# Optimization experiments

Measured on AMD Instinct MI355X. Metric: run time of the kernel, lower is better.

Reference implementation:

```python
import jax, jax.numpy as jnp
import numpy as np

NL, H, N, CIN, COUT, B, L = 4, 256, 64, 64, 8, 8, 1024
LN_EPS = 1e-5


def layernorm(x, w, b):
    m = x.mean(-1, keepdims=True)
    v = ((x - m) ** 2).mean(-1, keepdims=True)
    return (x - m) / jnp.sqrt(v + LN_EPS) * w + b


def s4d(u, A, C, D, log_step):
    # u: [B, H, L] real; A: [N] complex; C: [H, N] complex
    Lq = u.shape[-1]
    step = jnp.exp(log_step)                       # [H]
    dA = step[:, None] * A[None, :]                # [H, N] complex
    C_bar = C * (jnp.exp(dA) - 1.0) / A[None, :]   # [H, N]
    l = jnp.arange(Lq, dtype=jnp.float32)
    P = jnp.exp(l[:, None, None] * dA[None])       # [L, H, N] complex (dominant intermediate)
    K = jnp.einsum('hn,lhn->hl', C_bar, P)         # [H, L] complex
    kf = jnp.fft.rfft(K.real, n=2 * Lq) + 1j * jnp.fft.rfft(K.imag, n=2 * Lq)  # [H, L+1]
    uf = jnp.fft.rfft(u, n=2 * Lq)                 # [B, H, L+1]
    y = jnp.fft.irfft(kf * uf, n=2 * Lq)[..., :Lq]  # [B, H, L] real
    return y + u * D[:, None]


def forward(stimulus_seq, initial_state, A_re, A_im, C_re, C_im, D, log_step,
            ln1_w, ln1_b, ln2_w, ln2_b, W1, b1, W2, b2,
            Win, b_in, Wst, b_st, Wout, b_out):
    # stimulus_seq: [B, CIN, L] -> [B, L, CIN]
    x = stimulus_seq.transpose(0, 2, 1) @ Win.T + b_in            # [B, L, H]
    x = x + (initial_state @ Wst.T + b_st)[:, None, :]            # fusion_mode='add'
    for i in range(NL):
        xn = layernorm(x, ln1_w[i], ln1_b[i])
        A = A_re[i] + 1j * A_im[i]
        C = C_re[i] + 1j * C_im[i]
        y = s4d(xn.transpose(0, 2, 1), A, C, D[i], log_step[i])
        x = x + y.transpose(0, 2, 1)
        xn = layernorm(x, ln2_w[i], ln2_b[i])
        h = jax.nn.gelu(xn @ W1[i].T + b1[i], approximate=False)  # torch GELU = exact erf
        x = x + h @ W2[i].T + b2[i]
    out = x @ Wout.T + b_out                                      # [B, L, COUT]
    # use_voltage_filter=False: split + concat is identity on channel axis
    return out.transpose(0, 2, 1)                                 # [B, COUT, L]


def setup_inputs() -> dict:
    key = jax.random.key(0)
    ks = iter(jax.random.split(key, 24))
    def u(shape, fan_in):
        lim = 1.0 / np.sqrt(fan_in)
        return jax.random.uniform(next(ks), shape, minval=-lim, maxval=lim, dtype=jnp.float32)
    inp = {
        'stimulus_seq': jax.random.normal(next(ks), (B, CIN, L), dtype=jnp.float32),
        'initial_state': jax.random.normal(next(ks), (B, COUT), dtype=jnp.float32),
        'A_re': -0.5 * jnp.ones((NL, N), dtype=jnp.float32),
        'A_im': jnp.tile(jnp.arange(N, dtype=jnp.float32) * np.float32(np.pi), (NL, 1)),
        'C_re': jax.random.normal(next(ks), (NL, H, N), dtype=jnp.float32),
        'C_im': jax.random.normal(next(ks), (NL, H, N), dtype=jnp.float32),
        'D': jax.random.normal(next(ks), (NL, H), dtype=jnp.float32),
        'log_step': jax.random.uniform(next(ks), (NL, H), dtype=jnp.float32) * np.float32(np.log(0.1) - np.log(1e-4)) + np.float32(np.log(1e-4)),
        'ln1_w': jnp.ones((NL, H), dtype=jnp.float32),
        'ln1_b': jnp.zeros((NL, H), dtype=jnp.float32),
        'ln2_w': jnp.ones((NL, H), dtype=jnp.float32),
        'ln2_b': jnp.zeros((NL, H), dtype=jnp.float32),
        'W1': u((NL, 2 * H, H), H), 'b1': u((NL, 2 * H), H),
        'W2': u((NL, H, 2 * H), 2 * H), 'b2': u((NL, H), 2 * H),
        'Win': u((H, CIN), CIN), 'b_in': u((H,), CIN),
        'Wst': u((H, COUT), COUT), 'b_st': u((H,), COUT),
        'Wout': u((COUT, H), H), 'b_out': u((COUT,), H),
    }
    return inp


def reference(stimulus_seq, initial_state, A_re, A_im, C_re, C_im, D, log_step,
              ln1_w, ln1_b, ln2_w, ln2_b, W1, b1, W2, b2,
              Win, b_in, Wst, b_st, Wout, b_out):
    return forward(stimulus_seq, initial_state, A_re, A_im, C_re, C_im, D, log_step,
                   ln1_w, ln1_b, ln2_w, ln2_b, W1, b1, W2, b2,
                   Win, b_in, Wst, b_st, Wout, b_out)
```

## Files before the change

### kernel.cpp

```cpp
#include <hip/hip_runtime.h>
#include <math.h>

#define NL   4
#define H    256
#define NST  64
#define CIN  64
#define COUT 8
#define BB   8
#define LL   1024
#define NFFT 2048

typedef __attribute__((ext_vector_type(8))) short bf16x8;
typedef __attribute__((ext_vector_type(4))) short short4v;
typedef __attribute__((ext_vector_type(4))) int   int4v;
typedef __attribute__((ext_vector_type(4))) float f32x4;

__device__ __forceinline__ short f2bf(float f) {
  union { float f; unsigned u; } v; v.f = f;
  unsigned r = (v.u + 0x7fffu + ((v.u >> 16) & 1u)) >> 16;
  return (short)r;
}
__device__ __forceinline__ int IDX2(int a) { return a + (a >> 4); }
#define FBUF 2176

__device__ __forceinline__ float2 cadd(float2 a, float2 b) { return make_float2(a.x + b.x, a.y + b.y); }
__device__ __forceinline__ float2 csub(float2 a, float2 b) { return make_float2(a.x - b.x, a.y - b.y); }

template <int SGN>
__device__ __forceinline__ void bfly8(const float2 a[8], float2 A[8]) {
  const float RH = 0.70710678118654752f;
  float2 s0 = cadd(a[0], a[4]), s1 = csub(a[0], a[4]);
  float2 s2 = cadd(a[2], a[6]), s3 = csub(a[2], a[6]);
  float2 mi = (SGN < 0) ? make_float2(s3.y, -s3.x) : make_float2(-s3.y, s3.x);
  float2 E0 = cadd(s0, s2), E1 = cadd(s1, mi), E2 = csub(s0, s2), E3 = csub(s1, mi);
  float2 t0 = cadd(a[1], a[5]), t1 = csub(a[1], a[5]);
  float2 t2 = cadd(a[3], a[7]), t3 = csub(a[3], a[7]);
  float2 mj = (SGN < 0) ? make_float2(t3.y, -t3.x) : make_float2(-t3.y, t3.x);
  float2 O0 = cadd(t0, t2), O1 = cadd(t1, mj), O2 = csub(t0, t2), O3 = csub(t1, mj);
  float2 W0 = O0;
  float2 W1 = (SGN < 0) ? make_float2((O1.x + O1.y) * RH, (O1.y - O1.x) * RH)
                        : make_float2((O1.x - O1.y) * RH, (O1.x + O1.y) * RH);
  float2 W2 = (SGN < 0) ? make_float2(O2.y, -O2.x) : make_float2(-O2.y, O2.x);
  float2 W3 = (SGN < 0) ? make_float2((O3.y - O3.x) * RH, -(O3.x + O3.y) * RH)
                        : make_float2(-(O3.x + O3.y) * RH, (O3.x - O3.y) * RH);
  A[0] = cadd(E0, W0); A[4] = csub(E0, W0);
  A[1] = cadd(E1, W1); A[5] = csub(E1, W1);
  A[2] = cadd(E2, W2); A[6] = csub(E2, W2);
  A[3] = cadd(E3, W3); A[7] = csub(E3, W3);
}

template <int SGN>
__device__ __forceinline__ void fft_stage0_reg(const float2 a[8], float2* d,
                                               const float2* __restrict__ tw, int tid) {
  float2 A[8];
  bfly8<SGN>(a, A);
  const int base = 8 * tid;
  d[IDX2(base)] = A[0];
#pragma unroll
  for (int dd = 1; dd < 8; ++dd) {
    float2 w = tw[dd * tid];
    float wi = (SGN < 0) ? w.y : -w.y;
    d[IDX2(base + dd)] = make_float2(A[dd].x * w.x - A[dd].y * wi,
                                     A[dd].x * wi + A[dd].y * w.x);
  }
}

template <int SGN>
__device__ __forceinline__ void fft_stage0_reg_tw(const float2 a[8], float2* d,
                                                  const float2 w[7], int tid) {
  float2 A[8];
  bfly8<SGN>(a, A);
  const int base = 8 * tid;
  d[IDX2(base)] = A[0];
#pragma unroll
  for (int dd = 1; dd < 8; ++dd) {
    float wr = w[dd - 1].x;
    float wi = (SGN < 0) ? w[dd - 1].y : -w[dd - 1].y;
    d[IDX2(base + dd)] = make_float2(A[dd].x * wr - A[dd].y * wi,
                                     A[dd].x * wi + A[dd].y * wr);
  }
}

template <int SGN>
__device__ __forceinline__ void fft_mid_stages(float2* bA, float2* bB,
                                               const float2* __restrict__ tw, int tid) {
#pragma unroll
  for (int st = 1; st < 3; ++st) {
    float2* s = (st == 1) ? bA : bB;
    float2* d = (st == 1) ? bB : bA;
    const int m = 1 << (3 * st);
    __syncthreads();
    const int k  = tid & (m - 1);
    const int jm = tid - k;
    float2 a[8], A[8];
#pragma unroll
    for (int q = 0; q < 8; ++q) a[q] = s[IDX2(tid + 256 * q)];
    bfly8<SGN>(a, A);
    const int base = 8 * jm + k;
    d[IDX2(base)] = A[0];
#pragma unroll
    for (int dd = 1; dd < 8; ++dd) {
      float2 w = tw[dd * jm];
      float wi = (SGN < 0) ? w.y : -w.y;
      d[IDX2(base + dd * m)] = make_float2(A[dd].x * w.x - A[dd].y * wi,
                                           A[dd].x * wi + A[dd].y * w.x);
    }
  }
}

template <int SGN>
__device__ __forceinline__ void fft_final_r4_lds(const float2* s, float2* d, int tid) {
  __syncthreads();
#pragma unroll
  for (int q = 0; q < 2; ++q) {
    const int t = tid + (q << 8);
    float2 x0 = s[IDX2(t)], x1 = s[IDX2(t + 512)];
    float2 x2 = s[IDX2(t + 1024)], x3 = s[IDX2(t + 1536)];
    float2 s0 = cadd(x0, x2), s1 = csub(x0, x2);
    float2 s2 = cadd(x1, x3), s3 = csub(x1, x3);
    float2 mi = (SGN < 0) ? make_float2(s3.y, -s3.x) : make_float2(-s3.y, s3.x);
    d[IDX2(t)]        = cadd(s0, s2);
    d[IDX2(t + 512)]  = cadd(s1, mi);
    d[IDX2(t + 1024)] = csub(s0, s2);
    d[IDX2(t + 1536)] = csub(s1, mi);
  }
  __syncthreads();
}

template <int SGN>
__device__ __forceinline__ void fft_final_r4_reg(const float2* s, int tid,
                                                 float2 out0[4], float2 out1[4]) {
  __syncthreads();
#pragma unroll
  for (int q = 0; q < 2; ++q) {
    const int t = tid + (q << 8);
    float2 x0 = s[IDX2(t)], x1 = s[IDX2(t + 512)];
    float2 x2 = s[IDX2(t + 1024)], x3 = s[IDX2(t + 1536)];
    float2 s0 = cadd(x0, x2), s1 = csub(x0, x2);
    float2 s2 = cadd(x1, x3), s3 = csub(x1, x3);
    float2 mi = (SGN < 0) ? make_float2(s3.y, -s3.x) : make_float2(-s3.y, s3.x);
    float2* o = q ? out1 : out0;
    o[0] = cadd(s0, s2);
    o[1] = cadd(s1, mi);
    o[2] = csub(s0, s2);
    o[3] = csub(s1, mi);
  }
}

__global__ __launch_bounds__(256) void k_setup(
    const float* __restrict__ W1, const float* __restrict__ W2, const float* __restrict__ Win,
    const float* __restrict__ init, const float* __restrict__ Wst,
    const float* __restrict__ bst, const float* __restrict__ bin,
    short* __restrict__ W1s, short* __restrict__ W2s, float* __restrict__ WinT,
    float* __restrict__ sp, float2* __restrict__ tw) {
  int idx = blockIdx.x * 256 + threadIdx.x;
  if (idx < 2048) {
    float s, c;
    sincosf(3.14159265358979323846f * (float)idx / 1024.0f, &s, &c);
    tw[idx] = make_float2(c, -s);
  }
  if (idx < 65536) {
    int i = idx >> 14, c = idx & 16383;
    int cblk = c >> 11, s = (c >> 8) & 7, n = (c >> 6) & 3, lane = c & 63;
    int cl = lane & 15, rg = lane >> 4;
    int col = cblk * 64 + n * 16 + cl;
    const float* srcp = W1 + ((size_t)(i * 512 + col)) * 256 + s * 32 + rg * 8;
    short* dstp = W1s + ((size_t)idx) * 8;
#pragma unroll
    for (int j = 0; j < 8; ++j) dstp[j] = f2bf(srcp[j]);
  } else if (idx < 131072) {
    int t = idx - 65536;
    int i = t >> 14, c = t & 16383;
    int cblk = c >> 11, s = (c >> 7) & 15, n = (c >> 6) & 1, lane = c & 63;
    int cl = lane & 15, rg = lane >> 4;
    int col = cblk * 32 + n * 16 + cl;
    const float* srcp = W2 + ((size_t)(i * 256 + col)) * 512 + s * 32 + rg * 8;
    short* dstp = W2s + ((size_t)t) * 8;
#pragma unroll
    for (int j = 0; j < 8; ++j) dstp[j] = f2bf(srcp[j]);
  }
  if (idx < 256 * 64) {
    int hh = idx / 64, c = idx % 64;
    WinT[c * 256 + hh] = Win[idx];
  }
  if (idx < BB * H) {
    int b = idx >> 8, h = idx & 255;
    float acc = bin[h] + bst[h];
#pragma unroll
    for (int c = 0; c < COUT; ++c) acc += init[b * COUT + c] * Wst[h * COUT + c];
    sp[idx] = acc;
  }
}

__global__ __launch_bounds__(256) void k_in_ln1(
    const float* __restrict__ stim, const float* __restrict__ WinT,
    const float* __restrict__ sp, const float* __restrict__ lw, const float* __restrict__ lb,
    float* __restrict__ x, float* __restrict__ xnT) {
  int blk = blockIdx.x;
  int b_ = blk >> 6, l0 = (blk & 63) << 4;
  int tid = threadIdx.x, wv = tid >> 6, lane = tid & 63;
  __shared__ float sc[16][CIN];
  __shared__ float T[16][256];
#pragma unroll
  for (int it = 0; it < 4; ++it) {
    int idx = tid + (it << 8);
    int r = idx & 15, c = idx >> 4;
    sc[r][c] = stim[(b_ * CIN + c) * LL + l0 + r];
  }
  __syncthreads();
  float4 sp4 = *(const float4*)&sp[b_ * H + lane * 4];
  float4 acc[4] = {sp4, sp4, sp4, sp4};
  for (int c = 0; c < CIN; ++c) {
    float4 wv4 = *(const float4*)&WinT[c * H + lane * 4];
#pragma unroll
    for (int rr = 0; rr < 4; ++rr) {
      float s = sc[wv * 4 + rr][c];
      acc[rr].x += s * wv4.x; acc[rr].y += s * wv4.y;
      acc[rr].z += s * wv4.z; acc[rr].w += s * wv4.w;
    }
  }
  float4 w4 = *(const float4*)&lw[lane * 4];
  float4 c4 = *(const float4*)&lb[lane * 4];
#pragma unroll
  for (int rr = 0; rr < 4; ++rr) {
    int lr = wv * 4 + rr;
    float4 v = acc[rr];
    *(float4*)&x[(((size_t)(b_ << 10) + l0 + lr)) * H + lane * 4] = v;
    float s = v.x + v.y + v.z + v.w;
#pragma unroll
    for (int o = 32; o > 0; o >>= 1) s += __shfl_xor(s, o, 64);
    float m = s * (1.0f / H);
    float dx = v.x - m, dy = v.y - m, dz = v.z - m, dw = v.w - m;
    float q = dx * dx + dy * dy + dz * dz + dw * dw;
#pragma unroll
    for (int o = 32; o > 0; o >>= 1) q += __shfl_xor(q, o, 64);
    float rs = rsqrtf(q * (1.0f / H) + 1e-5f);
    float4 o4;
    o4.x = dx * rs * w4.x + c4.x; o4.y = dy * rs * w4.y + c4.y;
    o4.z = dz * rs * w4.z + c4.z; o4.w = dw * rs * w4.w + c4.w;
    *(float4*)&T[lr][lane * 4] = o4;
  }
  __syncthreads();
  float tmp[16];
#pragma unroll
  for (int l = 0; l < 16; ++l) tmp[l] = T[l][tid];
  float* dst = xnT + ((size_t)(b_ * H + tid)) * LL + l0;
#pragma unroll
  for (int l = 0; l < 16; l += 4) {
    float4 v = {tmp[l], tmp[l + 1], tmp[l + 2], tmp[l + 3]};
    *(float4*)&dst[l] = v;
  }
}

__global__ __launch_bounds__(256) void k_kernelfft(
    const float* __restrict__ A_re, const float* __restrict__ A_im,
    const float* __restrict__ C_re, const float* __restrict__ C_im,
    const float* __restrict__ log_step, const float2* __restrict__ tw,
    float2* __restrict__ kf) {
  int blk = blockIdx.x;
  int i = blk >> 8;
  int tid = threadIdx.x;
  __shared__ float2 cb[NST], Mv[NST];
  __shared__ float2 bufA[FBUF], bufB[FBUF];
  float2* T1 = bufB;
  float2* T2 = bufB + 1024;
  float step = expf(log_step[blk]);
  int n = tid & 63, g = tid >> 6;
  float Ar = A_re[i * NST + n], Ai = A_im[i * NST + n];
  float dr = step * Ar, di = step * Ai;
  float er = expf(dr);
  float sn, cs; sincosf(di, &sn, &cs);
  float Er = er * cs, Ei = er * sn;
  if (g == 0) {
    float nr = Er - 1.0f, ni = Ei;
    float dnm = Ar * Ar + Ai * Ai;
    float qr = (nr * Ar + ni * Ai) / dnm;
    float qi = (ni * Ar - nr * Ai) / dnm;
    float Cr = C_re[(size_t)blk * NST + n], Ci = C_im[(size_t)blk * NST + n];
    cb[n] = make_float2(Cr * qr - Ci * qi, Cr * qi + Ci * qr);
    float pr = 1.f, pi = 0.f;
    T1[n * 16] = make_float2(1.f, 0.f);
    for (int a = 1; a < 16; ++a) {
      float t2 = pr * Er - pi * Ei; pi = pr * Ei + pi * Er; pr = t2;
      T1[n * 16 + a] = make_float2(pr, pi);
    }
  } else if (g == 1) {
    float xr = Er, xi = Ei;
#pragma unroll
    for (int j = 0; j < 4; ++j) { float t2 = xr * xr - xi * xi; xi = 2.f * xr * xi; xr = t2; }
    float pr = 1.f, pi = 0.f;
    T2[n * 16] = make_float2(1.f, 0.f);
    for (int a = 1; a < 16; ++a) {
      float t2 = pr * xr - pi * xi; pi = pr * xi + pi * xr; pr = t2;
      T2[n * 16 + a] = make_float2(pr, pi);
    }
    float mr2 = pr * xr - pi * xi, mi2 = pr * xi + pi * xr;
    Mv[n] = make_float2(mr2, mi2);
  }
  __syncthreads();
  float kr[4] = {0.f, 0.f, 0.f, 0.f}, ki[4] = {0.f, 0.f, 0.f, 0.f};
  const int a_lo = tid & 15, a_hi = tid >> 4;
  for (int nn = 0; nn < NST; ++nn) {
    float2 t1 = T1[nn * 16 + a_lo];
    float2 t2v = T2[nn * 16 + a_hi];
    float pr = t1.x * t2v.x - t1.y * t2v.y;
    float pi = t1.x * t2v.y + t1.y * t2v.x;
    float2 c = cb[nn], m = Mv[nn];
#pragma unroll
    for (int q = 0; q < 4; ++q) {
      kr[q] += c.x * pr - c.y * pi;
      ki[q] += c.x * pi + c.y * pr;
      float t2 = pr * m.x - pi * m.y;
      pi = pr * m.y + pi * m.x;
      pr = t2;
    }
  }
  float2 a[8];
#pragma unroll
  for (int q = 0; q < 4; ++q) a[q] = make_float2(kr[q], ki[q]);
  a[4] = a[5] = a[6] = a[7] = make_float2(0.f, 0.f);
  fft_stage0_reg<-1>(a, bufA, tw, tid);
  fft_mid_stages<-1>(bufA, bufB, tw, tid);
  float2 F0[4], F1[4];
  fft_final_r4_reg<-1>(bufA, tid, F0, F1);
  float2* kfh = kf + (size_t)blk * 1025;
  kfh[tid]       = F0[0];
  kfh[tid + 512] = F0[1];
  kfh[tid + 256] = F1[0];
  kfh[tid + 768] = F1[1];
  if (tid == 0) kfh[1024] = F0[2];
}

__global__ __launch_bounds__(256) void k_conv(
    const float* __restrict__ xnT, const float2* __restrict__ kf,
    const float* __restrict__ D, const float2* __restrict__ tw, float* __restrict__ yT) {
  int blk = blockIdx.x;
  int b_ = blk >> 7, hp = blk & 127;
  int h0 = hp * 2, h1 = h0 + 1;
  int r0 = b_ * H + h0;
  int tid = threadIdx.x;
  __shared__ float2 bufA[FBUF], bufB[FBUF];
  float2 w0[7];
#pragma unroll
  for (int dd = 1; dd < 8; ++dd) w0[dd - 1] = tw[dd * tid];
  float u0[4], u1[4];
  const float* x0 = xnT + (size_t)r0 * LL;
  const float* x1 = x0 + LL;
  float2 a[8];
#pragma unroll
  for (int q = 0; q < 4; ++q) {
    int l = tid + (q << 8);
    float v0 = x0[l], v1 = x1[l];
    u0[q] = v0; u1[q] = v1;
    a[q] = make_float2(v0, v1);
  }
  a[4] = a[5] = a[6] = a[7] = make_float2(0.f, 0.f);
  fft_stage0_reg_tw<-1>(a, bufA, w0, tid);
  fft_mid_stages<-1>(bufA, bufB, tw, tid);
  fft_final_r4_lds<-1>(bufA, bufB, tid);
  const float2* kf0 = kf + (size_t)h0 * 1025;
  const float2* kf1 = kf + (size_t)h1 * 1025;
#pragma unroll
  for (int q = 0; q < 4; ++q) {
    int k = tid + (q << 8);
    if (k == 0) {
      float2 k0 = kf0[0], k1 = kf1[0];
      float2 F0 = bufB[IDX2(0)], Fn = bufB[IDX2(1024)];
      bufA[IDX2(0)]    = make_float2(F0.x * k0.x, F0.y * k1.x);
      float2 k0n = kf0[1024], k1n = kf1[1024];
      bufA[IDX2(1024)] = make_float2(Fn.x * k0n.x, Fn.y * k1n.x);
    } else {
      float2 F = bufB[IDX2(k)], G = bufB[IDX2(2048 - k)];
      float u0r = 0.5f * (F.x + G.x), u0i = 0.5f * (F.y - G.y);
      float dr_ = 0.5f * (F.x - G.x), di_ = 0.5f * (F.y + G.y);
      float u1r = di_, u1i = -dr_;
      float2 k0 = kf0[k], k1 = kf1[k];
      float z0r = u0r * k0.x - u0i * k0.y, z0i = u0r * k0.y + u0i * k0.x;
      float z1r = u1r * k1.x - u1i * k1.y, z1i = u1r * k1.y + u1i * k1.x;
      bufA[IDX2(k)]        = make_float2(z0r - z1i, z0i + z1r);
      bufA[IDX2(2048 - k)] = make_float2(z0r + z1i, z1r - z0i);
    }
  }
  __syncthreads();
  float2 g[8];
#pragma unroll
  for (int q = 0; q < 8; ++q) g[q] = bufA[IDX2(tid + 256 * q)];
  fft_stage0_reg_tw<1>(g, bufB, w0, tid);
  fft_mid_stages<1>(bufB, bufA, tw, tid);
  float2 z0[4], z1[4];
  fft_final_r4_reg<1>(bufB, tid, z0, z1);
  float Dh0 = D[h0], Dh1 = D[h1];
  float* y0 = yT + (size_t)r0 * LL;
  float* y1 = y0 + LL;
  const float s = 1.0f / NFFT;
  y0[tid]       = z0[0].x * s + Dh0 * u0[0];
  y0[tid + 256] = z1[0].x * s + Dh0 * u0[1];
  y0[tid + 512] = z0[1].x * s + Dh0 * u0[2];
  y0[tid + 768] = z1[1].x * s + Dh0 * u0[3];
  y1[tid]       = z0[0].y * s + Dh1 * u1[0];
  y1[tid + 256] = z1[0].y * s + Dh1 * u1[1];
  y1[tid + 512] = z0[1].y * s + Dh1 * u1[2];
  y1[tid + 768] = z1[1].y * s + Dh1 * u1[3];
}

#define TXS 260
template <bool LAST>
__global__ __launch_bounds__(512, 4) void k_mlp(
    const short* __restrict__ W1p, const float* __restrict__ b1p,
    const short* __restrict__ W2p, const float* __restrict__ b2p,
    float* __restrict__ x, const float* __restrict__ yT,
    const float* __restrict__ ln2w, const float* __restrict__ ln2b,
    const float* __restrict__ ln1w, const float* __restrict__ ln1b,
    float* __restrict__ xnT,
    const float* __restrict__ Wout, const float* __restrict__ bout,
    float* __restrict__ out) {
  const int m0 = blockIdx.x * 16;
  const int b_ = m0 >> 10, l0 = m0 & 1023;
  const int tid = threadIdx.x;
  const int lane = tid & 63, wid = tid >> 6;
  const int rg = lane >> 4, cl = lane & 15;
  __shared__ __attribute__((aligned(16))) char smem[26112];
  short* A1  = (short*)smem;
  short* A2  = (short*)(smem + 8448);
  float* red = (float*)(smem + 25088);
  float* Txn = (float*)smem;
  float* wlds = (float*)(smem + 16896);

  const short* w1base = W1p + (size_t)wid * 16384 + lane * 8;
  bf16x8 pre[4];
#pragma unroll
  for (int n = 0; n < 4; ++n)
    pre[n] = *(const bf16x8*)(w1base + n * 512);

  float v[2][4];
  float wl2[2], bl2[2];
#pragma unroll
  for (int n = 0; n < 2; ++n) {
    int col = wid * 32 + n * 16 + cl;
    wl2[n] = ln2w[col]; bl2[n] = ln2b[col];
  }
  float sum[4], sq[4];
#pragma unroll
  for (int r = 0; r < 4; ++r) { sum[r] = 0.f; sq[r] = 0.f; }
#pragma unroll
  for (int n = 0; n < 2; ++n) {
    int col = wid * 32 + n * 16 + cl;
    float4 y4 = *(const float4*)&yT[((size_t)(b_ * H + col)) * LL + l0 + rg * 4];
    float yv[4] = {y4.x, y4.y, y4.z, y4.w};
#pragma unroll
    for (int r = 0; r < 4; ++r) {
      int row = rg * 4 + r;
      float val = x[(size_t)(m0 + row) * H + col] + yv[r];
      v[n][r] = val;
      sum[r] += val; sq[r] += val * val;
    }
  }
#pragma unroll
  for (int r = 0; r < 4; ++r) {
#pragma unroll
    for (int o = 1; o < 16; o <<= 1) {
      sum[r] += __shfl_xor(sum[r], o, 64);
      sq[r]  += __shfl_xor(sq[r], o, 64);
    }
  }
  if (cl == 0) {
#pragma unroll
    for (int r = 0; r < 4; ++r) {
      int row = rg * 4 + r;
      red[(wid * 16 + row) * 2]     = sum[r];
      red[(wid * 16 + row) * 2 + 1] = sq[r];
    }
  }
  __syncthreads();
#pragma unroll
  for (int r = 0; r < 4; ++r) {
    int row = rg * 4 + r;
    float S = 0.f, Q = 0.f;
#pragma unroll
    for (int w = 0; w < 8; ++w) { S += red[(w * 16 + row) * 2]; Q += red[(w * 16 + row) * 2 + 1]; }
    float mean = S * (1.0f / H);
    float var = Q * (1.0f / H) - mean * mean;
    float rs = rsqrtf(var + 1e-5f);
#pragma unroll
    for (int n = 0; n < 2; ++n) {
      int col = wid * 32 + n * 16 + cl;
      A1[row * 264 + col] = f2bf((v[n][r] - mean) * rs * wl2[n] + bl2[n]);
    }
  }
  __syncthreads();

  f32x4 acc1[4];
#pragma unroll
  for (int n = 0; n < 4; ++n) acc1[n] = (f32x4){0.f, 0.f, 0.f, 0.f};
  {
#pragma unroll
    for (int s = 0; s < 8; ++s) {
      const int kk = s * 32;
      bf16x8 af, bfv[4];
      if (s == 0) {
#pragma unroll
        for (int n = 0; n < 4; ++n) bfv[n] = pre[n];
      } else {
#pragma unroll
        for (int n = 0; n < 4; ++n)
          bfv[n] = *(const bf16x8*)(w1base + (s * 4 + n) * 512);
      }
      af = *(const bf16x8*)&A1[cl * 264 + kk + rg * 8];
      __builtin_amdgcn_s_setprio(1);
#pragma unroll
      for (int n = 0; n < 4; ++n)
        acc1[n] = __builtin_amdgcn_mfma_f32_16x16x32_bf16(af, bfv[n], acc1[n], 0, 0, 0);
      __builtin_amdgcn_s_setprio(0);
    }
  }
#pragma unroll
  for (int n = 0; n < 4; ++n) {
    int col = wid * 64 + n * 16 + cl;
    float bb = b1p[col];
#pragma unroll
    for (int r = 0; r < 4; ++r) {
      int row = rg * 4 + r;
      float g = acc1[n][r] + bb;
      g = 0.5f * g * (1.0f + erff(g * 0.70710678118654752f));
      A2[row * 520 + col] = f2bf(g);
    }
  }
  __syncthreads();

  f32x4 acc2[2];
#pragma unroll
  for (int n = 0; n < 2; ++n) acc2[n] = (f32x4){0.f, 0.f, 0.f, 0.f};
  {
    const short* w2base = W2p + (size_t)wid * 16384 + lane * 8;
#pragma unroll
    for (int s = 0; s < 16; ++s) {
      const int kk = s * 32;
      bf16x8 af, bfv[2];
#pragma unroll
      for (int n = 0; n < 2; ++n)
        bfv[n] = *(const bf16x8*)(w2base + (s * 2 + n) * 512);
      af = *(const bf16x8*)&A2[cl * 520 + kk + rg * 8];
      __builtin_amdgcn_s_setprio(1);
#pragma unroll
      for (int n = 0; n < 2; ++n)
        acc2[n] = __builtin_amdgcn_mfma_f32_16x16x32_bf16(af, bfv[n], acc2[n], 0, 0, 0);
      __builtin_amdgcn_s_setprio(0);
    }
  }

  float bv[2], wl1[2], bl1[2];
#pragma unroll
  for (int n = 0; n < 2; ++n) {
    int col = wid * 32 + n * 16 + cl;
    bv[n] = b2p[col];
    if (!LAST) { wl1[n] = ln1w[col]; bl1[n] = ln1b[col]; }
  }
#pragma unroll
  for (int r = 0; r < 4; ++r) { sum[r] = 0.f; sq[r] = 0.f; }
#pragma unroll
  for (int n = 0; n < 2; ++n) {
#pragma unroll
    for (int r = 0; r < 4; ++r) {
      float vf = acc2[n][r] + bv[n] + v[n][r];
      acc2[n][r] = vf;
      sum[r] += vf; sq[r] += vf * vf;
    }
  }

  if (LAST) {
    __syncthreads();
#pragma unroll
    for (int n = 0; n < 2; ++n) {
      int col = wid * 32 + n * 16 + cl;
#pragma unroll
      for (int r = 0; r < 4; ++r) {
        int row = rg * 4 + r;
        Txn[row * TXS + col] = acc2[n][r];
      }
    }
#pragma unroll
    for (int it = 0; it < 4; ++it) {
      int idx = tid + (it << 9);
      wlds[(idx >> 8) * 258 + (idx & 255)] = Wout[idx];
    }
    __syncthreads();
    if (tid < 128) {
      int row = tid >> 3, co = tid & 7;
      float p = bout[co];
      const float* tr = Txn + row * TXS;
      const float* wr = wlds + co * 258;
#pragma unroll 4
      for (int c = 0; c < H; ++c) p += tr[c] * wr[c];
      out[((b_ * COUT + co) << 10) + l0 + row] = p;
    }
  } else {
#pragma unroll
    for (int r = 0; r < 4; ++r) {
#pragma unroll
      for (int o = 1; o < 16; o <<= 1) {
        sum[r] += __shfl_xor(sum[r], o, 64);
        sq[r]  += __shfl_xor(sq[r], o, 64);
      }
    }
    if (cl == 0) {
#pragma unroll
      for (int r = 0; r < 4; ++r) {
        int row = rg * 4 + r;
        red[(wid * 16 + row) * 2]     = sum[r];
        red[(wid * 16 + row) * 2 + 1] = sq[r];
      }
    }
    __syncthreads();
#pragma unroll
    for (int r = 0; r < 4; ++r) {
      int row = rg * 4 + r;
      float S = 0.f, Q = 0.f;
#pragma unroll
      for (int w = 0; w < 8; ++w) { S += red[(w * 16 + row) * 2]; Q += red[(w * 16 + row) * 2 + 1]; }
      float mean = S * (1.0f / H);
      float var = Q * (1.0f / H) - mean * mean;
      float rs = rsqrtf(var + 1e-5f);
#pragma unroll
      for (int n = 0; n < 2; ++n) {
        int col = wid * 32 + n * 16 + cl;
        float vf = acc2[n][r];
        x[(size_t)(m0 + row) * H + col] = vf;
        Txn[row * TXS + col] = (vf - mean) * rs * wl1[n] + bl1[n];
      }
    }
    __syncthreads();
    int h = tid & 255, seg = (tid >> 8) * 8;
    float tmp[8];
#pragma unroll
    for (int l = 0; l < 8; ++l) tmp[l] = Txn[(seg + l) * TXS + h];
    float* dst = xnT + ((size_t)(b_ * H + h)) * LL + l0 + seg;
#pragma unroll
    for (int l = 0; l < 8; l += 4) {
      float4 v4 = {tmp[l], tmp[l + 1], tmp[l + 2], tmp[l + 3]};
      *(float4*)&dst[l] = v4;
    }
  }
}

extern "C" void kernel_launch(void* const* d_in, const int* in_sizes, int n_in,
                              void* d_out, int out_size, void* d_ws, size_t ws_size,
                              hipStream_t stream) {
  const float* stim  = (const float*)d_in[0];
  const float* init  = (const float*)d_in[1];
  const float* A_re  = (const float*)d_in[2];
  const float* A_im  = (const float*)d_in[3];
  const float* C_re  = (const float*)d_in[4];
  const float* C_im  = (const float*)d_in[5];
  const float* Dp    = (const float*)d_in[6];
  const float* lstep = (const float*)d_in[7];
  const float* ln1w  = (const float*)d_in[8];
  const float* ln1b  = (const float*)d_in[9];
  const float* ln2w  = (const float*)d_in[10];
  const float* ln2b  = (const float*)d_in[11];
  const float* W1    = (const float*)d_in[12];
  const float* b1    = (const float*)d_in[13];
  const float* W2    = (const float*)d_in[14];
  const float* b2    = (const float*)d_in[15];
  const float* Win   = (const float*)d_in[16];
  const float* bin   = (const float*)d_in[17];
  const float* Wst   = (const float*)d_in[18];
  const float* bst   = (const float*)d_in[19];
  const float* Wout  = (const float*)d_in[20];
  const float* bout  = (const float*)d_in[21];
  float* out = (float*)d_out;
  float* ws = (float*)d_ws;

  size_t o = 0;
  auto alloc = [&](size_t nfloats) { size_t r = o; o += (nfloats + 63) & ~(size_t)63; return r; };
  float*  x    = ws + alloc((size_t)BB * LL * H);
  float*  xnT  = ws + alloc((size_t)BB * H * LL);
  float*  yT   = ws + alloc((size_t)BB * H * LL);
  float2* kf   = (float2*)(ws + alloc((size_t)NL * H * 1025 * 2));
  short*  W1s  = (short*)(ws + alloc((size_t)NL * 512 * 256 / 2));
  short*  W2s  = (short*)(ws + alloc((size_t)NL * 256 * 512 / 2));
  float*  WinT = ws + alloc((size_t)64 * 256);
  float*  sp   = ws + alloc((size_t)BB * H);
  float2* tw   = (float2*)(ws + alloc((size_t)2048 * 2));
  (void)ws_size; (void)in_sizes; (void)n_in; (void)out_size;

  k_setup<<<512, 256, 0, stream>>>(W1, W2, Win, init, Wst, bst, bin,
                                   W1s, W2s, WinT, sp, tw);
  k_kernelfft<<<NL * H, 256, 0, stream>>>(A_re, A_im, C_re, C_im, lstep, tw, kf);
  k_in_ln1<<<BB * 64, 256, 0, stream>>>(stim, WinT, sp, ln1w, ln1b, x, xnT);

  for (int i = 0; i < NL; ++i) {
    k_conv<<<BB * H / 2, 256, 0, stream>>>(xnT, kf + (size_t)i * H * 1025,
                                           Dp + i * H, tw, yT);
    if (i < NL - 1) {
      k_mlp<false><<<512, 512, 0, stream>>>(
          W1s + (size_t)i * 512 * 256, b1 + i * 512,
          W2s + (size_t)i * 256 * 512, b2 + i * H,
          x, yT, ln2w + i * H, ln2b + i * H,
          ln1w + (i + 1) * H, ln1b + (i + 1) * H, xnT,
          nullptr, nullptr, nullptr);
    } else {
      k_mlp<true><<<512, 512, 0, stream>>>(
          W1s + (size_t)i * 512 * 256, b1 + i * 512,
          W2s + (size_t)i * 256 * 512, b2 + i * H,
          x, yT, ln2w + i * H, ln2b + i * H,
          nullptr, nullptr, nullptr,
          Wout, bout, out);
    }
  }
}
```

Before: 180.5 us.

## Store residual stream and conv output in bf16; prefetch more MLP weights

The residual stream x and the S4D convolution output yT are now stored as bf16 instead of fp32, which halves the global traffic for these activations between k_in_ln1, k_conv and k_mlp. The MLP kernel also preloads the first two k-steps of W1 and W2 fragments into registers ahead of the matrix loops. The residual accumulation now loses precision at each of the four layers, which risks numerical drift. The larger set of preloaded registers may also raise register pressure under launch_bounds(512,4).

```diff
diff --git a/kernel.cpp b/kernel.cpp
--- a/kernel.cpp
+++ b/kernel.cpp
@@ -19,6 +19,11 @@
   union { float f; unsigned u; } v; v.f = f;
   unsigned r = (v.u + 0x7fffu + ((v.u >> 16) & 1u)) >> 16;
   return (short)r;
+}
+__device__ __forceinline__ float b2f(short s) {
+  union { unsigned u; float f; } v;
+  v.u = ((unsigned)(unsigned short)s) << 16;
+  return v.f;
 }
 __device__ __forceinline__ int IDX2(int a) { return a + (a >> 4); }
 #define FBUF 2176
@@ -195,7 +200,7 @@
 __global__ __launch_bounds__(256) void k_in_ln1(
     const float* __restrict__ stim, const float* __restrict__ WinT,
     const float* __restrict__ sp, const float* __restrict__ lw, const float* __restrict__ lb,
-    float* __restrict__ x, float* __restrict__ xnT) {
+    short* __restrict__ x, float* __restrict__ xnT) {
   int blk = blockIdx.x;
   int b_ = blk >> 6, l0 = (blk & 63) << 4;
   int tid = threadIdx.x, wv = tid >> 6, lane = tid & 63;
@@ -225,7 +230,9 @@
   for (int rr = 0; rr < 4; ++rr) {
     int lr = wv * 4 + rr;
     float4 v = acc[rr];
-    *(float4*)&x[(((size_t)(b_ << 10) + l0 + lr)) * H + lane * 4] = v;
+    short4v s4;
+    s4[0] = f2bf(v.x); s4[1] = f2bf(v.y); s4[2] = f2bf(v.z); s4[3] = f2bf(v.w);
+    *(short4v*)&x[(((size_t)(b_ << 10) + l0 + lr)) * H + lane * 4] = s4;
     float s = v.x + v.y + v.z + v.w;
 #pragma unroll
     for (int o = 32; o > 0; o >>= 1) s += __shfl_xor(s, o, 64);
@@ -333,7 +340,7 @@
 
 __global__ __launch_bounds__(256) void k_conv(
     const float* __restrict__ xnT, const float2* __restrict__ kf,
-    const float* __restrict__ D, const float2* __restrict__ tw, float* __restrict__ yT) {
+    const float* __restrict__ D, const float2* __restrict__ tw, short* __restrict__ yT) {
   int blk = blockIdx.x;
   int b_ = blk >> 7, hp = blk & 127;
   int h0 = hp * 2, h1 = h0 + 1;
@@ -390,17 +397,17 @@
   float2 z0[4], z1[4];
   fft_final_r4_reg<1>(bufB, tid, z0, z1);
   float Dh0 = D[h0], Dh1 = D[h1];
-  float* y0 = yT + (size_t)r0 * LL;
-  float* y1 = y0 + LL;
+  short* y0 = yT + (size_t)r0 * LL;
+  short* y1 = y0 + LL;
   const float s = 1.0f / NFFT;
-  y0[tid]       = z0[0].x * s + Dh0 * u0[0];
-  y0[tid + 256] = z1[0].x * s + Dh0 * u0[1];
-  y0[tid + 512] = z0[1].x * s + Dh0 * u0[2];
-  y0[tid + 768] = z1[1].x * s + Dh0 * u0[3];
-  y1[tid]       = z0[0].y * s + Dh1 * u1[0];
-  y1[tid + 256] = z1[0].y * s + Dh1 * u1[1];
-  y1[tid + 512] = z0[1].y * s + Dh1 * u1[2];
-  y1[tid + 768] = z1[1].y * s + Dh1 * u1[3];
+  y0[tid]       = f2bf(z0[0].x * s + Dh0 * u0[0]);
+  y0[tid + 256] = f2bf(z1[0].x * s + Dh0 * u0[1]);
+  y0[tid + 512] = f2bf(z0[1].x * s + Dh0 * u0[2]);
+  y0[tid + 768] = f2bf(z1[1].x * s + Dh0 * u0[3]);
+  y1[tid]       = f2bf(z0[0].y * s + Dh1 * u1[0]);
+  y1[tid + 256] = f2bf(z1[0].y * s + Dh1 * u1[1]);
+  y1[tid + 512] = f2bf(z0[1].y * s + Dh1 * u1[2]);
+  y1[tid + 768] = f2bf(z1[1].y * s + Dh1 * u1[3]);
 }
 
 #define TXS 260
@@ -408,7 +415,7 @@
 __global__ __launch_bounds__(512, 4) void k_mlp(
     const short* __restrict__ W1p, const float* __restrict__ b1p,
     const short* __restrict__ W2p, const float* __restrict__ b2p,
-    float* __restrict__ x, const float* __restrict__ yT,
+    short* __restrict__ x, const short* __restrict__ yT,
     const float* __restrict__ ln2w, const float* __restrict__ ln2b,
     const float* __restrict__ ln1w, const float* __restrict__ ln1b,
     float* __restrict__ xnT,
@@ -427,9 +434,10 @@
   float* wlds = (float*)(smem + 16896);
 
   const short* w1base = W1p + (size_t)wid * 16384 + lane * 8;
-  bf16x8 pre[4];
-#pragma unroll
-  for (int n = 0; n < 4; ++n)
+  const short* w2base = W2p + (size_t)wid * 16384 + lane * 8;
+  bf16x8 pre[8];
+#pragma unroll
+  for (int n = 0; n < 8; ++n)
     pre[n] = *(const bf16x8*)(w1base + n * 512);
 
   float v[2][4];
@@ -445,12 +453,12 @@
 #pragma unroll
   for (int n = 0; n < 2; ++n) {
     int col = wid * 32 + n * 16 + cl;
-    float4 y4 = *(const float4*)&yT[((size_t)(b_ * H + col)) * LL + l0 + rg * 4];
-    float yv[4] = {y4.x, y4.y, y4.z, y4.w};
+    short4v y4 = *(const short4v*)&yT[((size_t)(b_ * H + col)) * LL + l0 + rg * 4];
+    float yv[4] = {b2f(y4[0]), b2f(y4[1]), b2f(y4[2]), b2f(y4[3])};
 #pragma unroll
     for (int r = 0; r < 4; ++r) {
       int row = rg * 4 + r;
-      float val = x[(size_t)(m0 + row) * H + col] + yv[r];
+      float val = b2f(x[(size_t)(m0 + row) * H + col]) + yv[r];
       v[n][r] = val;
       sum[r] += val; sq[r] += val * val;
     }
@@ -497,9 +505,9 @@
     for (int s = 0; s < 8; ++s) {
       const int kk = s * 32;
       bf16x8 af, bfv[4];
-      if (s == 0) {
-#pragma unroll
-        for (int n = 0; n < 4; ++n) bfv[n] = pre[n];
+      if (s < 2) {
+#pragma unroll
+        for (int n = 0; n < 4; ++n) bfv[n] = pre[s * 4 + n];
       } else {
 #pragma unroll
         for (int n = 0; n < 4; ++n)
@@ -513,6 +521,10 @@
       __builtin_amdgcn_s_setprio(0);
     }
   }
+  bf16x8 pre2[4];
+#pragma unroll
+  for (int n = 0; n < 4; ++n)
+    pre2[n] = *(const bf16x8*)(w2base + n * 512);
 #pragma unroll
   for (int n = 0; n < 4; ++n) {
     int col = wid * 64 + n * 16 + cl;
@@ -531,14 +543,18 @@
 #pragma unroll
   for (int n = 0; n < 2; ++n) acc2[n] = (f32x4){0.f, 0.f, 0.f, 0.f};
   {
-    const short* w2base = W2p + (size_t)wid * 16384 + lane * 8;
 #pragma unroll
     for (int s = 0; s < 16; ++s) {
       const int kk = s * 32;
       bf16x8 af, bfv[2];
-#pragma unroll
-      for (int n = 0; n < 2; ++n)
-        bfv[n] = *(const bf16x8*)(w2base + (s * 2 + n) * 512);
+      if (s < 2) {
+#pragma unroll
+        for (int n = 0; n < 2; ++n) bfv[n] = pre2[s * 2 + n];
+      } else {
+#pragma unroll
+        for (int n = 0; n < 2; ++n)
+          bfv[n] = *(const bf16x8*)(w2base + (s * 2 + n) * 512);
+      }
       af = *(const bf16x8*)&A2[cl * 520 + kk + rg * 8];
       __builtin_amdgcn_s_setprio(1);
 #pragma unroll
@@ -624,7 +640,7 @@
       for (int n = 0; n < 2; ++n) {
         int col = wid * 32 + n * 16 + cl;
         float vf = acc2[n][r];
-        x[(size_t)(m0 + row) * H + col] = vf;
+        x[(size_t)(m0 + row) * H + col] = f2bf(vf);
         Txn[row * TXS + col] = (vf - mean) * rs * wl1[n] + bl1[n];
       }
     }
@@ -672,9 +688,9 @@
 
   size_t o = 0;
   auto alloc = [&](size_t nfloats) { size_t r = o; o += (nfloats + 63) & ~(size_t)63; return r; };
-  float*  x    = ws + alloc((size_t)BB * LL * H);
+  short*  x    = (short*)(ws + alloc((size_t)BB * LL * H / 2));
   float*  xnT  = ws + alloc((size_t)BB * H * LL);
-  float*  yT   = ws + alloc((size_t)BB * H * LL);
+  short*  yT   = (short*)(ws + alloc((size_t)BB * H * LL / 2));
   float2* kf   = (float2*)(ws + alloc((size_t)NL * H * 1025 * 2));
   short*  W1s  = (short*)(ws + alloc((size_t)NL * 512 * 256 / 2));
   short*  W2s  = (short*)(ws + alloc((size_t)NL * 256 * 512 / 2));
```

Measured after the change: 175.9 us (median of 2 runs). 2.6% less time.
